# Optimization experiments

Hardware: AMD Instinct MI355X
Metric: run time of the kernel (lower is better)

## Reference

```python
import jax, jax.numpy as jnp
import numpy as np

V, E, H, L = 32000, 512, 1024, 2
B, S = 16, 128


def _gru_cell(x, h, w_ih, w_hh, b_ih, b_hh):
    # PyTorch GRUCell: gates ordered (r, z, n), chunks of size H
    gi = x @ w_ih.T + b_ih            # (B, 3H)
    gh = h @ w_hh.T + b_hh            # (B, 3H)
    i_r, i_z, i_n = jnp.split(gi, 3, axis=-1)
    h_r, h_z, h_n = jnp.split(gh, 3, axis=-1)
    r = jax.nn.sigmoid(i_r + h_r)
    z = jax.nn.sigmoid(i_z + h_z)
    n = jnp.tanh(i_n + r * h_n)
    return (1.0 - z) * n + z * h


def setup_inputs() -> dict:
    key = jax.random.key(0)
    ks = jax.random.split(key, 16)
    s = lambda fan: 1.0 / np.sqrt(fan)
    inp = {
        "hidden": jax.random.normal(ks[0], (L, B, H), jnp.float32),
        "trg": jax.random.randint(ks[1], (B, S), 0, V),
        "embedding": jax.random.normal(ks[2], (V, E), jnp.float32) * 0.02,
        # layer 0 GRU (input_size=E)
        "w_ih0": jax.random.uniform(ks[3], (3 * H, E), jnp.float32, -s(H), s(H)),
        "w_hh0": jax.random.uniform(ks[4], (3 * H, H), jnp.float32, -s(H), s(H)),
        "b_ih0": jnp.zeros((3 * H,), jnp.float32),
        "b_hh0": jnp.zeros((3 * H,), jnp.float32),
        # layer 1 GRU (input_size=H)
        "w_ih1": jax.random.uniform(ks[5], (3 * H, H), jnp.float32, -s(H), s(H)),
        "w_hh1": jax.random.uniform(ks[6], (3 * H, H), jnp.float32, -s(H), s(H)),
        "b_ih1": jnp.zeros((3 * H,), jnp.float32),
        "b_hh1": jnp.zeros((3 * H,), jnp.float32),
        # output projection MLP: Linear(H,H) -> ReLU -> Linear(H,E)
        "w1": jax.random.uniform(ks[7], (H, H), jnp.float32, -s(H), s(H)),
        "b1": jnp.zeros((H,), jnp.float32),
        "w2": jax.random.uniform(ks[8], (E, H), jnp.float32, -s(H), s(H)),
        "b2": jnp.zeros((E,), jnp.float32),
        # generator bias (weight tied to embedding)
        "b_gen": jnp.zeros((V,), jnp.float32),
    }
    return inp


def reference(hidden, trg, embedding, w_ih0, w_hh0, b_ih0, b_hh0,
              w_ih1, w_hh1, b_ih1, b_hh1, w1, b1, w2, b2, b_gen):
    def step(h, tok):
        # h: (L, B, H); tok: (B,)
        x = embedding[tok]                                 # (B, E)
        h0 = _gru_cell(x, h[0], w_ih0, w_hh0, b_ih0, b_hh0)
        h1 = _gru_cell(h0, h[1], w_ih1, w_hh1, b_ih1, b_hh1)
        new_h = jnp.stack([h0, h1], axis=0)
        out = jax.nn.relu(h1 @ w1.T + b1) @ w2.T + b2      # (B, E)
        logit = out @ embedding.T + b_gen                  # (B, V) weight-tied
        return new_h, logit

    _, logits = jax.lax.scan(step, hidden, trg.T)          # (S, B, V)
    return jnp.transpose(logits, (1, 0, 2))                # (B, S, V)
```

## Files before the change

### kernel.cpp

```cpp
#include <hip/hip_runtime.h>
#include <math.h>

#define Sn 128
#define Bn 16
#define Hn 1024
#define En 512
#define Vn 32000
#define H3 3072
#define NL0 32
#define NL1 64

typedef _Float16 h16;
typedef __attribute__((ext_vector_type(4))) _Float16 h16x4;
typedef __attribute__((ext_vector_type(8))) _Float16 h16x8;
typedef __attribute__((ext_vector_type(4))) float f32x4;

#define Q_EMB   4096000
#define Q_WIH0  (Q_EMB + 393216)
#define Q_W1    (Q_WIH0 + 262144)
#define Q_W2    (Q_W1 + 131072)
#define Q_WHH0  (Q_W2 + 786432)
#define Q_WIH1  (Q_WHH0 + 786432)
#define Q_WHH1  (Q_WIH1 + 786432)
#define Q_HID   (Q_WHH1 + 8192)
__global__ __launch_bounds__(256) void cvt_all_k(
    const float* __restrict__ emb, const float* __restrict__ wih0,
    const float* __restrict__ w1, const float* __restrict__ w2,
    const float* __restrict__ whh0, const float* __restrict__ wih1,
    const float* __restrict__ whh1, const float* __restrict__ hid,
    h16* __restrict__ E, h16* __restrict__ A, h16* __restrict__ B1,
    h16* __restrict__ B2, h16* __restrict__ D0, h16* __restrict__ D1,
    h16* __restrict__ D2, h16* __restrict__ HD)
{
  int i = blockIdx.x * 256 + threadIdx.x;
  const float* s; h16* d; int o;
  if      (i < Q_EMB)  { s = emb;  d = E;  o = i; }
  else if (i < Q_WIH0) { s = wih0; d = A;  o = i - Q_EMB; }
  else if (i < Q_W1)   { s = w1;   d = B1; o = i - Q_WIH0; }
  else if (i < Q_W2)   { s = w2;   d = B2; o = i - Q_W1; }
  else if (i < Q_WHH0) { s = whh0; d = D0; o = i - Q_W2; }
  else if (i < Q_WIH1) { s = wih1; d = D1; o = i - Q_WHH0; }
  else if (i < Q_WHH1) { s = whh1; d = D2; o = i - Q_WIH1; }
  else                 { s = hid;  d = HD; o = i - Q_WHH1; }
  float4 v = *(const float4*)(s + (size_t)o * 4);
  h16x4 ov = { (h16)v.x, (h16)v.y, (h16)v.z, (h16)v.w };
  *(h16x4*)(d + (size_t)o * 4) = ov;
}

__global__ void embed_k(const int* __restrict__ trg, const float* __restrict__ emb,
                        h16* __restrict__ Xh) {
  int t = blockIdx.x;
  int s = t >> 4, b = t & 15;
  int tok = trg[b * Sn + s];
  const float* src = emb + (size_t)tok * En;
  int e = threadIdx.x * 4;
  float4 v = *(const float4*)(src + e);
  h16x4 o = { (h16)v.x, (h16)v.y, (h16)v.z, (h16)v.w };
  *(h16x4*)(Xh + (size_t)t * En + e) = o;
}

template<int OUT_MODE, bool RELU, bool SWZ>
__global__ __launch_bounds__(256) void gemm_bt(
    const h16* __restrict__ A, const h16* __restrict__ B,
    const float* __restrict__ bias, void* __restrict__ C,
    int M, int N, int K)
{
  __shared__ h16 As[128 * 64];
  __shared__ h16 Bs[128 * 64];
  int tid = threadIdx.x;
  int l = tid & 63, wv = tid >> 6;
  int wr = wv >> 1, wc = wv & 1;

  int work = blockIdx.x;
  if (SWZ) { int q = gridDim.x >> 3; work = (work & 7) * q + (work >> 3); }
  int nMp = M >> 7;
  int brow = (work % nMp) << 7;
  int bcol = (work / nMp) << 7;

  f32x4 acc[4][4];
#pragma unroll
  for (int m = 0; m < 4; ++m)
#pragma unroll
    for (int n = 0; n < 4; ++n) acc[m][n] = (f32x4){0.f, 0.f, 0.f, 0.f};

  int nkt = K >> 6;
  for (int kt = 0; kt < nkt; ++kt) {
    const h16* Ag = A + (size_t)brow * K + kt * 64;
    const h16* Bg = B + (size_t)bcol * K + kt * 64;
#pragma unroll
    for (int c = tid; c < 2048; c += 256) {
      int half = c >> 10;
      int cc = c & 1023;
      int row = cc >> 3, slot = cc & 7;
      const h16* src = (half ? Bg : Ag) + (size_t)row * K + slot * 8;
      uint4 v = *(const uint4*)src;
      h16* dst = (half ? Bs : As) + row * 64 + ((slot ^ (row & 7)) << 3);
      *(uint4*)dst = v;
    }
    __syncthreads();
#pragma unroll
    for (int kk = 0; kk < 2; ++kk) {
      h16x8 af[4], bfr[4];
      int rb = wr * 64 + (l & 15);
      int cb2 = wc * 64 + (l & 15);
      int slot = kk * 4 + (l >> 4);
#pragma unroll
      for (int m = 0; m < 4; ++m) {
        int r = rb + m * 16;
        af[m] = *(const h16x8*)&As[r * 64 + ((slot ^ (r & 7)) << 3)];
      }
#pragma unroll
      for (int n = 0; n < 4; ++n) {
        int r = cb2 + n * 16;
        bfr[n] = *(const h16x8*)&Bs[r * 64 + ((slot ^ (r & 7)) << 3)];
      }
#pragma unroll
      for (int m = 0; m < 4; ++m)
#pragma unroll
        for (int n = 0; n < 4; ++n)
          acc[m][n] = __builtin_amdgcn_mfma_f32_16x16x32_f16(af[m], bfr[n], acc[m][n], 0, 0, 0);
    }
    __syncthreads();
  }

#pragma unroll
  for (int m = 0; m < 4; ++m) {
    int row0 = brow + wr * 64 + m * 16 + ((l >> 4) << 2);
#pragma unroll
    for (int n = 0; n < 4; ++n) {
      int col = bcol + wc * 64 + n * 16 + (l & 15);
      float bv = bias ? bias[col] : 0.f;
#pragma unroll
      for (int i = 0; i < 4; ++i) {
        int row = row0 + i;
        float v = acc[m][n][i] + bv;
        if (RELU) v = fmaxf(v, 0.f);
        if (OUT_MODE == 1) {
          ((h16*)C)[(size_t)row * N + col] = (h16)v;
        } else if (OUT_MODE == 2) {
          int rr = ((row & 15) << 7) + (row >> 4);
          ((float*)C)[(size_t)rr * N + col] = v;
        } else {
          ((float*)C)[(size_t)row * N + col] = v;
        }
      }
    }
  }
}

__global__ __launch_bounds__(256, 1) void gemm_bt256(
    const h16* __restrict__ A, const h16* __restrict__ B,
    const float* __restrict__ bias, float* __restrict__ C,
    int M, int N, int K)
{
  __shared__ h16 As[128 * 64];
  __shared__ h16 Bs[256 * 64];
  int tid = threadIdx.x;
  int l = tid & 63, wv = tid >> 6;
  int wr = wv >> 1, wc = wv & 1;

  int work = blockIdx.x;
  int q = gridDim.x >> 3; work = (work & 7) * q + (work >> 3);
  int nMp = M >> 7;
  int brow = (work % nMp) << 7;
  int bcol = (work / nMp) << 8;

  f32x4 acc[4][8];
#pragma unroll
  for (int m = 0; m < 4; ++m)
#pragma unroll
    for (int n = 0; n < 8; ++n) acc[m][n] = (f32x4){0.f, 0.f, 0.f, 0.f};

  int nkt = K >> 6;
  for (int kt = 0; kt < nkt; ++kt) {
    const h16* Ag = A + (size_t)brow * K + kt * 64;
    const h16* Bg = B + (size_t)bcol * K + kt * 64;
#pragma unroll
    for (int c = tid; c < 3072; c += 256) {
      int isB = (c >= 1024);
      int cc = isB ? (c - 1024) : c;
      int row = cc >> 3, slot = cc & 7;
      const h16* src = (isB ? Bg : Ag) + (size_t)row * K + slot * 8;
      uint4 v = *(const uint4*)src;
      h16* dst = (isB ? Bs : As) + row * 64 + ((slot ^ (row & 7)) << 3);
      *(uint4*)dst = v;
    }
    __syncthreads();
#pragma unroll
    for (int kk = 0; kk < 2; ++kk) {
      h16x8 af[4], bfr[8];
      int rb = wr * 64 + (l & 15);
      int cb2 = wc * 128 + (l & 15);
      int slot = kk * 4 + (l >> 4);
#pragma unroll
      for (int m = 0; m < 4; ++m) {
        int r = rb + m * 16;
        af[m] = *(const h16x8*)&As[r * 64 + ((slot ^ (r & 7)) << 3)];
      }
#pragma unroll
      for (int n = 0; n < 8; ++n) {
        int r = cb2 + n * 16;
        bfr[n] = *(const h16x8*)&Bs[r * 64 + ((slot ^ (r & 7)) << 3)];
      }
#pragma unroll
      for (int m = 0; m < 4; ++m)
#pragma unroll
        for (int n = 0; n < 8; ++n)
          acc[m][n] = __builtin_amdgcn_mfma_f32_16x16x32_f16(af[m], bfr[n], acc[m][n], 0, 0, 0);
    }
    __syncthreads();
  }

#pragma unroll
  for (int m = 0; m < 4; ++m) {
    int row0 = brow + wr * 64 + m * 16 + ((l >> 4) << 2);
#pragma unroll
    for (int n = 0; n < 8; ++n) {
      int col = bcol + wc * 128 + n * 16 + (l & 15);
      float bv = bias[col];
#pragma unroll
      for (int i = 0; i < 4; ++i) {
        int row = row0 + i;
        int rr = ((row & 15) << 7) + (row >> 4);
        C[(size_t)rr * N + col] = acc[m][n][i] + bv;
      }
    }
  }
}

__global__ __launch_bounds__(384, 1) void gru_mfma(
    const float* __restrict__ gi0,
    const float* __restrict__ hidden,
    const h16* __restrict__ hinit16,
    const h16* __restrict__ whh0, const float* __restrict__ bhh0,
    const h16* __restrict__ wih1, const float* __restrict__ bih1,
    const h16* __restrict__ whh1, const float* __restrict__ bhh1,
    h16* __restrict__ h0ring,
    h16* __restrict__ H1A,
    int* __restrict__ flags)
{
  __shared__ float exch[5][256];
  int bid = blockIdx.x;
  int tid = threadIdx.x;
  int w = tid >> 6, l = tid & 63;
  int li = l & 15;
  int ko = (l >> 4) << 3;
  int b0 = (l >> 4) << 2;

  __threadfence();

  int* fL0 = flags;
  int* fL1 = flags + 1024;

  if (bid < NL0) {
    int gate = w >> 1, ch = w & 1;
    int j = bid * 32 + ch * 16 + li;
    h16x8 Bf[32];
    {
      const h16* wp = whh0 + ((size_t)((gate << 10) + j) << 10) + ko;
#pragma unroll
      for (int t = 0; t < 32; ++t) Bf[t] = *(const h16x8*)(wp + t * 32);
    }
    float bR = 0.f, bZ = 0.f, bN = 0.f;
    float hprev[4];
    if (gate == 2) {
      bR = bhh0[j]; bZ = bhh0[1024 + j]; bN = bhh0[2048 + j];
#pragma unroll
      for (int i = 0; i < 4; ++i) hprev[i] = hidden[((b0 + i) << 10) + j];
    }

    for (int s = 0; s < Sn; ++s) {
      if (s > 0) {
        if (w == 0 && l < NL0)
          while (__hip_atomic_load(&fL0[l << 5], __ATOMIC_RELAXED, __HIP_MEMORY_SCOPE_AGENT) < s) {}
        __syncthreads();
        asm volatile("" ::: "memory");
      }
      float gr[4], gz[4], gn[4];
      if (gate == 2) {
        const float* gb = gi0 + ((size_t)s << 4) * H3;
#pragma unroll
        for (int i = 0; i < 4; ++i) {
          const float* g = gb + (size_t)(b0 + i) * H3 + j;
          gr[i] = g[0]; gz[i] = g[1024]; gn[i] = g[2048];
        }
      }
      const h16* hsrc = (s == 0) ? hinit16 : h0ring + (((size_t)(s - 1)) << 14);
      const h16* Ap = hsrc + (li << 10) + ko;
      f32x4 acc = (f32x4){0.f, 0.f, 0.f, 0.f};
#pragma unroll
      for (int t = 0; t < 32; ++t)
        acc = __builtin_amdgcn_mfma_f32_16x16x32_f16(*(const h16x8*)(Ap + t * 32), Bf[t], acc, 0, 0, 0);
      if (w < 4) {
#pragma unroll
        for (int i = 0; i < 4; ++i) exch[w][((b0 + i) << 4) + li] = acc[i];
      }
      __syncthreads();
      if (gate == 2) {
#pragma unroll
        for (int i = 0; i < 4; ++i) {
          int e = ((b0 + i) << 4) + li;
          float r = 1.f / (1.f + expf(-(exch[ch][e] + bR + gr[i])));
          float z = 1.f / (1.f + expf(-(exch[2 + ch][e] + bZ + gz[i])));
          float n = tanhf(gn[i] + r * (acc[i] + bN));
          float out = (1.f - z) * n + z * hprev[i];
          hprev[i] = out;
          h16 hv = (h16)out; unsigned short us; __builtin_memcpy(&us, &hv, 2);
          __hip_atomic_store((unsigned short*)h0ring + (((size_t)s) << 14) + ((b0 + i) << 10) + j,
                             us, __ATOMIC_RELAXED, __HIP_MEMORY_SCOPE_AGENT);
        }
      }
      __syncthreads();
      if (tid == 0)
        __hip_atomic_store(&fL0[bid << 5], s + 1, __ATOMIC_RELAXED, __HIP_MEMORY_SCOPE_AGENT);
    }
  } else {
    int bl = bid - NL0;
    int j = (bl << 4) + li;
    int isHH = (w >= 3);
    int gate = isHH ? (w - 3) : w;
    h16x8 Bf[32];
    {
      const h16* wsrc = isHH ? whh1 : wih1;
      const h16* wp = wsrc + ((size_t)((gate << 10) + j) << 10) + ko;
#pragma unroll
      for (int t = 0; t < 32; ++t) Bf[t] = *(const h16x8*)(wp + t * 32);
    }
    float bIR = 0.f, bIZ = 0.f, bIN = 0.f, bHR = 0.f, bHZ = 0.f, bHN = 0.f;
    float hprev[4];
    if (w == 5) {
      bIR = bih1[j]; bIZ = bih1[1024 + j]; bIN = bih1[2048 + j];
      bHR = bhh1[j]; bHZ = bhh1[1024 + j]; bHN = bhh1[2048 + j];
#pragma unroll
      for (int i = 0; i < 4; ++i) hprev[i] = hidden[16384 + ((b0 + i) << 10) + j];
    }

    for (int s = 1; s <= Sn; ++s) {
      if (w == 0) {
        if (l < NL0)
          while (__hip_atomic_load(&fL0[l << 5], __ATOMIC_RELAXED, __HIP_MEMORY_SCOPE_AGENT) < s) {}
      } else if (w == 1 && s >= 2) {
        while (__hip_atomic_load(&fL1[l << 5], __ATOMIC_RELAXED, __HIP_MEMORY_SCOPE_AGENT) < s) {}
      }
      __syncthreads();
      asm volatile("" ::: "memory");
      const h16* hsrc = isHH
          ? ((s == 1) ? hinit16 + 16384 : H1A + (((size_t)(s - 2)) << 14))
          : (h0ring + (((size_t)(s - 1)) << 14));
      const h16* Ap = hsrc + (li << 10) + ko;
      f32x4 acc = (f32x4){0.f, 0.f, 0.f, 0.f};
#pragma unroll
      for (int t = 0; t < 32; ++t)
        acc = __builtin_amdgcn_mfma_f32_16x16x32_f16(*(const h16x8*)(Ap + t * 32), Bf[t], acc, 0, 0, 0);
      if (w < 5) {
#pragma unroll
        for (int i = 0; i < 4; ++i) exch[w][((b0 + i) << 4) + li] = acc[i];
      }
      __syncthreads();
      if (w == 5) {
#pragma unroll
        for (int i = 0; i < 4; ++i) {
          int e = ((b0 + i) << 4) + li;
          float r = 1.f / (1.f + expf(-(exch[0][e] + bIR + exch[3][e] + bHR)));
          float z = 1.f / (1.f + expf(-(exch[1][e] + bIZ + exch[4][e] + bHZ)));
          float n = tanhf(exch[2][e] + bIN + r * (acc[i] + bHN));
          float out = (1.f - z) * n + z * hprev[i];
          hprev[i] = out;
          h16 hv = (h16)out; unsigned short us; __builtin_memcpy(&us, &hv, 2);
          __hip_atomic_store((unsigned short*)H1A + (((size_t)(s - 1)) << 14) + ((b0 + i) << 10) + j,
                             us, __ATOMIC_RELAXED, __HIP_MEMORY_SCOPE_AGENT);
        }
      }
      __syncthreads();
      if (tid == 0)
        __hip_atomic_store(&fL1[bl << 5], s + 1, __ATOMIC_RELAXED, __HIP_MEMORY_SCOPE_AGENT);
    }
  }
}

extern "C" void kernel_launch(void* const* d_in, const int* in_sizes, int n_in,
                              void* d_out, int out_size, void* d_ws, size_t ws_size,
                              hipStream_t stream) {
  const float* hidden = (const float*)d_in[0];
  const int*   trg    = (const int*)d_in[1];
  const float* emb    = (const float*)d_in[2];
  const float* w_ih0  = (const float*)d_in[3];
  const float* w_hh0  = (const float*)d_in[4];
  const float* b_ih0  = (const float*)d_in[5];
  const float* b_hh0  = (const float*)d_in[6];
  const float* w_ih1  = (const float*)d_in[7];
  const float* w_hh1  = (const float*)d_in[8];
  const float* b_ih1  = (const float*)d_in[9];
  const float* b_hh1  = (const float*)d_in[10];
  const float* w1     = (const float*)d_in[11];
  const float* b1     = (const float*)d_in[12];
  const float* w2     = (const float*)d_in[13];
  const float* b2     = (const float*)d_in[14];
  const float* b_gen  = (const float*)d_in[15];

  char* ws = (char*)d_ws;
  size_t off = 0;
  float* GI0    = (float*)(ws + off); off += (size_t)Sn * Bn * H3 * 4;
  h16* Xh       = (h16*)(ws + off);   off += (size_t)Sn * Bn * En * 2;
  h16* embH     = (h16*)(ws + off);   off += (size_t)Vn * En * 2;
  h16* wih0H    = (h16*)(ws + off);   off += (size_t)H3 * En * 2;
  h16* w1H      = (h16*)(ws + off);   off += (size_t)Hn * Hn * 2;
  h16* w2H      = (h16*)(ws + off);   off += (size_t)En * Hn * 2;
  h16* whh0H    = (h16*)(ws + off);   off += (size_t)H3 * Hn * 2;
  h16* wih1H    = (h16*)(ws + off);   off += (size_t)H3 * Hn * 2;
  h16* whh1H    = (h16*)(ws + off);   off += (size_t)H3 * Hn * 2;
  h16* H1A      = (h16*)(ws + off);   off += (size_t)Sn * Bn * Hn * 2;
  h16* h0ring   = (h16*)(ws + off);   off += (size_t)Sn * Bn * Hn * 2;
  h16* hinit16  = (h16*)(ws + off);   off += (size_t)2 * Bn * Hn * 2;
  int* flags    = (int*)(ws + off);   off += 16384;
  h16* Tb = (h16*)GI0;
  h16* Ub = (h16*)((char*)GI0 + (8u << 20));

  cvt_all_k<<<28320, 256, 0, stream>>>(emb, w_ih0, w1, w2, w_hh0, w_ih1, w_hh1, hidden,
                                       embH, wih0H, w1H, w2H, whh0H, wih1H, whh1H, hinit16);
  embed_k<<<Sn * Bn, 128, 0, stream>>>(trg, emb, Xh);

  gemm_bt<0, false, true><<<384, 256, 0, stream>>>(Xh, wih0H, b_ih0, GI0, Sn * Bn, H3, En);

  (void)hipMemsetAsync(flags, 0, 16384, stream);
  gru_mfma<<<NL0 + NL1, 384, 0, stream>>>(GI0, hidden, hinit16,
                                          whh0H, b_hh0, wih1H, b_ih1, whh1H, b_hh1,
                                          h0ring, H1A, flags);

  gemm_bt<1, true,  true><<<128,  256, 0, stream>>>(H1A, w1H, b1, Tb, Sn * Bn, Hn, Hn);
  gemm_bt<1, false, true><<<64,   256, 0, stream>>>(Tb, w2H, b2, Ub, Sn * Bn, En, Hn);
  gemm_bt256<<<2000, 256, 0, stream>>>(Ub, embH, b_gen, (float*)d_out, Sn * Bn, Vn, En);
}
```

Baseline: 1.488 ms.

## Fuse GRU recurrence and output head into one persistent megakernel with flag-based overlap

Merges the recurrent GRU kernel and the three head GEMMs (MLP layers and tied-embedding logits) into a single launch. Extra blocks wait on per-step layer-1 flags and per-chunk counters, so each 128-row chunk (8 timesteps) of the head computation can start while the recurrence is still running. Tb and Ub get dedicated workspace buffers instead of aliasing GI0, which is still being read. The design relies on the 96 recurrent blocks being co-resident with the spinning head blocks and on the head blocks being dispatched roughly in order. It also gives up the larger-grid GEMM tiling and runs the head GEMMs on 384-thread blocks where only 4 of the 6 waves compute.

```diff
diff --git a/kernel.cpp b/kernel.cpp
--- a/kernel.cpp
+++ b/kernel.cpp
@@ -137,9 +137,6 @@
         if (RELU) v = fmaxf(v, 0.f);
         if (OUT_MODE == 1) {
           ((h16*)C)[(size_t)row * N + col] = (h16)v;
-        } else if (OUT_MODE == 2) {
-          int rr = ((row & 15) << 7) + (row >> 4);
-          ((float*)C)[(size_t)rr * N + col] = v;
         } else {
           ((float*)C)[(size_t)row * N + col] = v;
         }
@@ -148,233 +145,354 @@
   }
 }
 
-__global__ __launch_bounds__(256, 1) void gemm_bt256(
-    const h16* __restrict__ A, const h16* __restrict__ B,
-    const float* __restrict__ bias, float* __restrict__ C,
-    int M, int N, int K)
+
+__device__ __forceinline__ void wait_fL1(int* fL1, int target, int tid) {
+  if (tid < 64) {
+    for (;;) {
+      int v = __hip_atomic_load(&fL1[tid << 5], __ATOMIC_RELAXED, __HIP_MEMORY_SCOPE_AGENT);
+      if (__all(v >= target)) break;
+      __builtin_amdgcn_s_sleep(8);
+    }
+  }
+  __syncthreads();
+  asm volatile("" ::: "memory");
+}
+
+__device__ __forceinline__ void wait_cnt(int* c, int target, int tid) {
+  if (tid == 0) {
+    while (__hip_atomic_load(c, __ATOMIC_RELAXED, __HIP_MEMORY_SCOPE_AGENT) < target)
+      __builtin_amdgcn_s_sleep(8);
+  }
+  __syncthreads();
+  asm volatile("" ::: "memory");
+}
+
+__device__ __forceinline__ void publish_cnt(int* c) {
+  __syncthreads();
+  if (threadIdx.x == 0) {
+    __threadfence();
+    atomicAdd(c, 1);
+  }
+}
+
+__device__ __forceinline__ void gemm_head128(
+    const h16* __restrict__ A, const h16* __restrict__ B, const float* __restrict__ bias,
+    h16* __restrict__ C, int ldc, int K, int relu, char* dyn, int tid)
 {
-  __shared__ h16 As[128 * 64];
-  __shared__ h16 Bs[256 * 64];
-  int tid = threadIdx.x;
+  h16* As = (h16*)dyn;
+  h16* Bs = (h16*)(dyn + 16384);
   int l = tid & 63, wv = tid >> 6;
   int wr = wv >> 1, wc = wv & 1;
-
-  int work = blockIdx.x;
-  int q = gridDim.x >> 3; work = (work & 7) * q + (work >> 3);
-  int nMp = M >> 7;
-  int brow = (work % nMp) << 7;
-  int bcol = (work / nMp) << 8;
-
-  f32x4 acc[4][8];
+  f32x4 acc[4][4];
 #pragma unroll
   for (int m = 0; m < 4; ++m)
 #pragma unroll
-    for (int n = 0; n < 8; ++n) acc[m][n] = (f32x4){0.f, 0.f, 0.f, 0.f};
-
+    for (int n = 0; n < 4; ++n) acc[m][n] = (f32x4){0.f, 0.f, 0.f, 0.f};
   int nkt = K >> 6;
   for (int kt = 0; kt < nkt; ++kt) {
-    const h16* Ag = A + (size_t)brow * K + kt * 64;
-    const h16* Bg = B + (size_t)bcol * K + kt * 64;
-#pragma unroll
-    for (int c = tid; c < 3072; c += 256) {
+    const h16* Ag = A + kt * 64;
+    const h16* Bg = B + kt * 64;
+    for (int c = tid; c < 2048; c += 384) {
+      int half = c >> 10, cc = c & 1023, row = cc >> 3, slot = cc & 7;
+      const h16* src = (half ? Bg : Ag) + (size_t)row * K + slot * 8;
+      uint4 v = *(const uint4*)src;
+      h16* dst = (half ? Bs : As) + row * 64 + ((slot ^ (row & 7)) << 3);
+      *(uint4*)dst = v;
+    }
+    __syncthreads();
+    if (wv < 4) {
+#pragma unroll
+      for (int kk = 0; kk < 2; ++kk) {
+        h16x8 af[4], bfr[4];
+        int rb = wr * 64 + (l & 15);
+        int cb2 = wc * 64 + (l & 15);
+        int slot = kk * 4 + (l >> 4);
+#pragma unroll
+        for (int m = 0; m < 4; ++m) {
+          int r = rb + m * 16;
+          af[m] = *(const h16x8*)&As[r * 64 + ((slot ^ (r & 7)) << 3)];
+        }
+#pragma unroll
+        for (int n = 0; n < 4; ++n) {
+          int r = cb2 + n * 16;
+          bfr[n] = *(const h16x8*)&Bs[r * 64 + ((slot ^ (r & 7)) << 3)];
+        }
+#pragma unroll
+        for (int m = 0; m < 4; ++m)
+#pragma unroll
+          for (int n = 0; n < 4; ++n)
+            acc[m][n] = __builtin_amdgcn_mfma_f32_16x16x32_f16(af[m], bfr[n], acc[m][n], 0, 0, 0);
+      }
+    }
+    __syncthreads();
+  }
+  if (wv < 4) {
+#pragma unroll
+    for (int m = 0; m < 4; ++m) {
+      int row0 = wr * 64 + m * 16 + ((l >> 4) << 2);
+#pragma unroll
+      for (int n = 0; n < 4; ++n) {
+        int col = wc * 64 + n * 16 + (l & 15);
+        float bv = bias[col];
+#pragma unroll
+        for (int i = 0; i < 4; ++i) {
+          float v = acc[m][n][i] + bv;
+          if (relu) v = fmaxf(v, 0.f);
+          C[(size_t)(row0 + i) * ldc + col] = (h16)v;
+        }
+      }
+    }
+  }
+}
+
+__device__ __forceinline__ void gemm_headlogit(
+    const h16* __restrict__ A, const h16* __restrict__ B, const float* __restrict__ bias,
+    float* __restrict__ C, int growbase, char* dyn, int tid)
+{
+  h16* As = (h16*)dyn;
+  h16* Bs = (h16*)(dyn + 16384);
+  int l = tid & 63, wv = tid >> 6;
+  int wr = wv >> 1, wc = wv & 1;
+  f32x4 acc[4][8];
+#pragma unroll
+  for (int m = 0; m < 4; ++m)
+#pragma unroll
+    for (int n = 0; n < 8; ++n) acc[m][n] = (f32x4){0.f, 0.f, 0.f, 0.f};
+  for (int kt = 0; kt < 8; ++kt) {
+    const h16* Ag = A + kt * 64;
+    const h16* Bg = B + kt * 64;
+    for (int c = tid; c < 3072; c += 384) {
       int isB = (c >= 1024);
       int cc = isB ? (c - 1024) : c;
       int row = cc >> 3, slot = cc & 7;
-      const h16* src = (isB ? Bg : Ag) + (size_t)row * K + slot * 8;
+      const h16* src = (isB ? Bg : Ag) + (size_t)row * 512 + slot * 8;
       uint4 v = *(const uint4*)src;
       h16* dst = (isB ? Bs : As) + row * 64 + ((slot ^ (row & 7)) << 3);
       *(uint4*)dst = v;
     }
     __syncthreads();
-#pragma unroll
-    for (int kk = 0; kk < 2; ++kk) {
-      h16x8 af[4], bfr[8];
-      int rb = wr * 64 + (l & 15);
-      int cb2 = wc * 128 + (l & 15);
-      int slot = kk * 4 + (l >> 4);
-#pragma unroll
-      for (int m = 0; m < 4; ++m) {
-        int r = rb + m * 16;
-        af[m] = *(const h16x8*)&As[r * 64 + ((slot ^ (r & 7)) << 3)];
-      }
+    if (wv < 4) {
+#pragma unroll
+      for (int kk = 0; kk < 2; ++kk) {
+        h16x8 af[4], bfr[8];
+        int rb = wr * 64 + (l & 15);
+        int cb2 = wc * 128 + (l & 15);
+        int slot = kk * 4 + (l >> 4);
+#pragma unroll
+        for (int m = 0; m < 4; ++m) {
+          int r = rb + m * 16;
+          af[m] = *(const h16x8*)&As[r * 64 + ((slot ^ (r & 7)) << 3)];
+        }
+#pragma unroll
+        for (int n = 0; n < 8; ++n) {
+          int r = cb2 + n * 16;
+          bfr[n] = *(const h16x8*)&Bs[r * 64 + ((slot ^ (r & 7)) << 3)];
+        }
+#pragma unroll
+        for (int m = 0; m < 4; ++m)
+#pragma unroll
+          for (int n = 0; n < 8; ++n)
+            acc[m][n] = __builtin_amdgcn_mfma_f32_16x16x32_f16(af[m], bfr[n], acc[m][n], 0, 0, 0);
+      }
+    }
+    __syncthreads();
+  }
+  if (wv < 4) {
+#pragma unroll
+    for (int m = 0; m < 4; ++m) {
+      int row0 = wr * 64 + m * 16 + ((l >> 4) << 2);
 #pragma unroll
       for (int n = 0; n < 8; ++n) {
-        int r = cb2 + n * 16;
-        bfr[n] = *(const h16x8*)&Bs[r * 64 + ((slot ^ (r & 7)) << 3)];
-      }
-#pragma unroll
-      for (int m = 0; m < 4; ++m)
-#pragma unroll
-        for (int n = 0; n < 8; ++n)
-          acc[m][n] = __builtin_amdgcn_mfma_f32_16x16x32_f16(af[m], bfr[n], acc[m][n], 0, 0, 0);
-    }
-    __syncthreads();
-  }
-
-#pragma unroll
-  for (int m = 0; m < 4; ++m) {
-    int row0 = brow + wr * 64 + m * 16 + ((l >> 4) << 2);
-#pragma unroll
-    for (int n = 0; n < 8; ++n) {
-      int col = bcol + wc * 128 + n * 16 + (l & 15);
-      float bv = bias[col];
-#pragma unroll
-      for (int i = 0; i < 4; ++i) {
-        int row = row0 + i;
-        int rr = ((row & 15) << 7) + (row >> 4);
-        C[(size_t)rr * N + col] = acc[m][n][i] + bv;
-      }
-    }
-  }
-}
-
-__global__ __launch_bounds__(384, 1) void gru_mfma(
+        int col = wc * 128 + n * 16 + (l & 15);
+        float bv = bias[col];
+#pragma unroll
+        for (int i = 0; i < 4; ++i) {
+          int grow = growbase + row0 + i;
+          int rr = ((grow & 15) << 7) + (grow >> 4);
+          C[(size_t)rr * Vn + col] = acc[m][n][i] + bv;
+        }
+      }
+    }
+  }
+}
+
+__global__ __launch_bounds__(384) void mega(
     const float* __restrict__ gi0,
     const float* __restrict__ hidden,
     const h16* __restrict__ hinit16,
     const h16* __restrict__ whh0, const float* __restrict__ bhh0,
     const h16* __restrict__ wih1, const float* __restrict__ bih1,
     const h16* __restrict__ whh1, const float* __restrict__ bhh1,
-    h16* __restrict__ h0ring,
-    h16* __restrict__ H1A,
-    int* __restrict__ flags)
+    h16* __restrict__ h0ring, h16* __restrict__ H1A,
+    int* __restrict__ flags,
+    const h16* __restrict__ w1H, const float* __restrict__ b1, h16* __restrict__ Tb,
+    const h16* __restrict__ w2H, const float* __restrict__ b2, h16* __restrict__ Ub,
+    const h16* __restrict__ embH, const float* __restrict__ b_gen,
+    float* __restrict__ out)
 {
-  __shared__ float exch[5][256];
+  extern __shared__ char dyn[];
   int bid = blockIdx.x;
   int tid = threadIdx.x;
-  int w = tid >> 6, l = tid & 63;
-  int li = l & 15;
-  int ko = (l >> 4) << 3;
-  int b0 = (l >> 4) << 2;
 
   __threadfence();
 
-  int* fL0 = flags;
-  int* fL1 = flags + 1024;
-
-  if (bid < NL0) {
-    int gate = w >> 1, ch = w & 1;
-    int j = bid * 32 + ch * 16 + li;
-    h16x8 Bf[32];
-    {
-      const h16* wp = whh0 + ((size_t)((gate << 10) + j) << 10) + ko;
-#pragma unroll
-      for (int t = 0; t < 32; ++t) Bf[t] = *(const h16x8*)(wp + t * 32);
-    }
-    float bR = 0.f, bZ = 0.f, bN = 0.f;
-    float hprev[4];
-    if (gate == 2) {
-      bR = bhh0[j]; bZ = bhh0[1024 + j]; bN = bhh0[2048 + j];
-#pragma unroll
-      for (int i = 0; i < 4; ++i) hprev[i] = hidden[((b0 + i) << 10) + j];
-    }
-
-    for (int s = 0; s < Sn; ++s) {
-      if (s > 0) {
-        if (w == 0 && l < NL0)
-          while (__hip_atomic_load(&fL0[l << 5], __ATOMIC_RELAXED, __HIP_MEMORY_SCOPE_AGENT) < s) {}
+  int* fL0  = flags;
+  int* fL1  = flags + 1024;
+  int* cnt1 = flags + 3072;
+  int* cnt2 = flags + 3328;
+
+  if (bid < NL0 + NL1) {
+    float* exch = (float*)dyn;
+    int w = tid >> 6, l = tid & 63;
+    int li = l & 15;
+    int ko = (l >> 4) << 3;
+    int b0 = (l >> 4) << 2;
+
+    if (bid < NL0) {
+      int gate = w >> 1, ch = w & 1;
+      int j = bid * 32 + ch * 16 + li;
+      h16x8 Bf[32];
+      {
+        const h16* wp = whh0 + ((size_t)((gate << 10) + j) << 10) + ko;
+#pragma unroll
+        for (int t = 0; t < 32; ++t) Bf[t] = *(const h16x8*)(wp + t * 32);
+      }
+      float bR = 0.f, bZ = 0.f, bN = 0.f;
+      float hprev[4];
+      if (gate == 2) {
+        bR = bhh0[j]; bZ = bhh0[1024 + j]; bN = bhh0[2048 + j];
+#pragma unroll
+        for (int i = 0; i < 4; ++i) hprev[i] = hidden[((b0 + i) << 10) + j];
+      }
+      for (int s = 0; s < Sn; ++s) {
+        if (s > 0) {
+          if (w == 0 && l < NL0)
+            while (__hip_atomic_load(&fL0[l << 5], __ATOMIC_RELAXED, __HIP_MEMORY_SCOPE_AGENT) < s) {}
+          __syncthreads();
+          asm volatile("" ::: "memory");
+        }
+        float gr[4], gz[4], gn[4];
+        if (gate == 2) {
+          const float* gb = gi0 + ((size_t)s << 4) * H3;
+#pragma unroll
+          for (int i = 0; i < 4; ++i) {
+            const float* g = gb + (size_t)(b0 + i) * H3 + j;
+            gr[i] = g[0]; gz[i] = g[1024]; gn[i] = g[2048];
+          }
+        }
+        const h16* hsrc = (s == 0) ? hinit16 : h0ring + (((size_t)(s - 1)) << 14);
+        const h16* Ap = hsrc + (li << 10) + ko;
+        f32x4 acc = (f32x4){0.f, 0.f, 0.f, 0.f};
+#pragma unroll
+        for (int t = 0; t < 32; ++t)
+          acc = __builtin_amdgcn_mfma_f32_16x16x32_f16(*(const h16x8*)(Ap + t * 32), Bf[t], acc, 0, 0, 0);
+        if (w < 4) {
+#pragma unroll
+          for (int i = 0; i < 4; ++i) exch[w * 256 + ((b0 + i) << 4) + li] = acc[i];
+        }
+        __syncthreads();
+        if (gate == 2) {
+#pragma unroll
+          for (int i = 0; i < 4; ++i) {
+            int e = ((b0 + i) << 4) + li;
+            float r = 1.f / (1.f + expf(-(exch[ch * 256 + e] + bR + gr[i])));
+            float z = 1.f / (1.f + expf(-(exch[(2 + ch) * 256 + e] + bZ + gz[i])));
+            float n = tanhf(gn[i] + r * (acc[i] + bN));
+            float o = (1.f - z) * n + z * hprev[i];
+            hprev[i] = o;
+            h16 hv = (h16)o; unsigned short us; __builtin_memcpy(&us, &hv, 2);
+            __hip_atomic_store((unsigned short*)h0ring + (((size_t)s) << 14) + ((b0 + i) << 10) + j,
+                               us, __ATOMIC_RELAXED, __HIP_MEMORY_SCOPE_AGENT);
+          }
+        }
+        __syncthreads();
+        if (tid == 0)
+          __hip_atomic_store(&fL0[bid << 5], s + 1, __ATOMIC_RELAXED, __HIP_MEMORY_SCOPE_AGENT);
+      }
+    } else {
+      int bl = bid - NL0;
+      int j = (bl << 4) + li;
+      int isHH = (w >= 3);
+      int gate = isHH ? (w - 3) : w;
+      h16x8 Bf[32];
+      {
+        const h16* wsrc = isHH ? whh1 : wih1;
+        const h16* wp = wsrc + ((size_t)((gate << 10) + j) << 10) + ko;
+#pragma unroll
+        for (int t = 0; t < 32; ++t) Bf[t] = *(const h16x8*)(wp + t * 32);
+      }
+      float bIR = 0.f, bIZ = 0.f, bIN = 0.f, bHR = 0.f, bHZ = 0.f, bHN = 0.f;
+      float hprev[4];
+      if (w == 5) {
+        bIR = bih1[j]; bIZ = bih1[1024 + j]; bIN = bih1[2048 + j];
+        bHR = bhh1[j]; bHZ = bhh1[1024 + j]; bHN = bhh1[2048 + j];
+#pragma unroll
+        for (int i = 0; i < 4; ++i) hprev[i] = hidden[16384 + ((b0 + i) << 10) + j];
+      }
+      for (int s = 1; s <= Sn; ++s) {
+        if (w == 0) {
+          if (l < NL0)
+            while (__hip_atomic_load(&fL0[l << 5], __ATOMIC_RELAXED, __HIP_MEMORY_SCOPE_AGENT) < s) {}
+        } else if (w == 1 && s >= 2) {
+          while (__hip_atomic_load(&fL1[l << 5], __ATOMIC_RELAXED, __HIP_MEMORY_SCOPE_AGENT) < s) {}
+        }
         __syncthreads();
         asm volatile("" ::: "memory");
-      }
-      float gr[4], gz[4], gn[4];
-      if (gate == 2) {
-        const float* gb = gi0 + ((size_t)s << 4) * H3;
-#pragma unroll
-        for (int i = 0; i < 4; ++i) {
-          const float* g = gb + (size_t)(b0 + i) * H3 + j;
-          gr[i] = g[0]; gz[i] = g[1024]; gn[i] = g[2048];
-        }
-      }
-      const h16* hsrc = (s == 0) ? hinit16 : h0ring + (((size_t)(s - 1)) << 14);
-      const h16* Ap = hsrc + (li << 10) + ko;
-      f32x4 acc = (f32x4){0.f, 0.f, 0.f, 0.f};
-#pragma unroll
-      for (int t = 0; t < 32; ++t)
-        acc = __builtin_amdgcn_mfma_f32_16x16x32_f16(*(const h16x8*)(Ap + t * 32), Bf[t], acc, 0, 0, 0);
-      if (w < 4) {
-#pragma unroll
-        for (int i = 0; i < 4; ++i) exch[w][((b0 + i) << 4) + li] = acc[i];
-      }
-      __syncthreads();
-      if (gate == 2) {
-#pragma unroll
-        for (int i = 0; i < 4; ++i) {
-          int e = ((b0 + i) << 4) + li;
-          float r = 1.f / (1.f + expf(-(exch[ch][e] + bR + gr[i])));
-          float z = 1.f / (1.f + expf(-(exch[2 + ch][e] + bZ + gz[i])));
-          float n = tanhf(gn[i] + r * (acc[i] + bN));
-          float out = (1.f - z) * n + z * hprev[i];
-          hprev[i] = out;
-          h16 hv = (h16)out; unsigned short us; __builtin_memcpy(&us, &hv, 2);
-          __hip_atomic_store((unsigned short*)h0ring + (((size_t)s) << 14) + ((b0 + i) << 10) + j,
-                             us, __ATOMIC_RELAXED, __HIP_MEMORY_SCOPE_AGENT);
-        }
-      }
-      __syncthreads();
-      if (tid == 0)
-        __hip_atomic_store(&fL0[bid << 5], s + 1, __ATOMIC_RELAXED, __HIP_MEMORY_SCOPE_AGENT);
-    }
+        const h16* hsrc = isHH
+            ? ((s == 1) ? hinit16 + 16384 : H1A + (((size_t)(s - 2)) << 14))
+            : (h0ring + (((size_t)(s - 1)) << 14));
+        const h16* Ap = hsrc + (li << 10) + ko;
+        f32x4 acc = (f32x4){0.f, 0.f, 0.f, 0.f};
+#pragma unroll
+        for (int t = 0; t < 32; ++t)
+          acc = __builtin_amdgcn_mfma_f32_16x16x32_f16(*(const h16x8*)(Ap + t * 32), Bf[t], acc, 0, 0, 0);
+        if (w < 5) {
+#pragma unroll
+          for (int i = 0; i < 4; ++i) exch[w * 256 + ((b0 + i) << 4) + li] = acc[i];
+        }
+        __syncthreads();
+        if (w == 5) {
+#pragma unroll
+          for (int i = 0; i < 4; ++i) {
+            int e = ((b0 + i) << 4) + li;
+            float r = 1.f / (1.f + expf(-(exch[e] + bIR + exch[768 + e] + bHR)));
+            float z = 1.f / (1.f + expf(-(exch[256 + e] + bIZ + exch[1024 + e] + bHZ)));
+            float n = tanhf(exch[512 + e] + bIN + r * (acc[i] + bHN));
+            float o = (1.f - z) * n + z * hprev[i];
+            hprev[i] = o;
+            h16 hv = (h16)o; unsigned short us; __builtin_memcpy(&us, &hv, 2);
+            __hip_atomic_store((unsigned short*)H1A + (((size_t)(s - 1)) << 14) + ((b0 + i) << 10) + j,
+                               us, __ATOMIC_RELAXED, __HIP_MEMORY_SCOPE_AGENT);
+          }
+        }
+        __syncthreads();
+        if (tid == 0)
+          __hip_atomic_store(&fL1[bl << 5], s + 1, __ATOMIC_RELAXED, __HIP_MEMORY_SCOPE_AGENT);
+      }
+    }
+    return;
+  }
+
+  int hb = bid - (NL0 + NL1);
+  int m = hb / 137;
+  int r = hb - m * 137;
+
+  if (r < 8) {
+    wait_fL1(fL1, 8 * m + 9, tid);
+    gemm_head128(H1A + (size_t)(m * 128) * Hn, w1H + (size_t)(r * 128) * Hn,
+                 b1 + r * 128, Tb + (size_t)(m * 128) * Hn + r * 128, Hn, Hn, 1, dyn, tid);
+    publish_cnt(&cnt1[m << 3]);
+  } else if (r < 12) {
+    int rn = r - 8;
+    wait_cnt(&cnt1[m << 3], 8, tid);
+    gemm_head128(Tb + (size_t)(m * 128) * Hn, w2H + (size_t)(rn * 128) * Hn,
+                 b2 + rn * 128, Ub + (size_t)(m * 128) * En + rn * 128, En, Hn, 0, dyn, tid);
+    publish_cnt(&cnt2[m << 3]);
   } else {
-    int bl = bid - NL0;
-    int j = (bl << 4) + li;
-    int isHH = (w >= 3);
-    int gate = isHH ? (w - 3) : w;
-    h16x8 Bf[32];
-    {
-      const h16* wsrc = isHH ? whh1 : wih1;
-      const h16* wp = wsrc + ((size_t)((gate << 10) + j) << 10) + ko;
-#pragma unroll
-      for (int t = 0; t < 32; ++t) Bf[t] = *(const h16x8*)(wp + t * 32);
-    }
-    float bIR = 0.f, bIZ = 0.f, bIN = 0.f, bHR = 0.f, bHZ = 0.f, bHN = 0.f;
-    float hprev[4];
-    if (w == 5) {
-      bIR = bih1[j]; bIZ = bih1[1024 + j]; bIN = bih1[2048 + j];
-      bHR = bhh1[j]; bHZ = bhh1[1024 + j]; bHN = bhh1[2048 + j];
-#pragma unroll
-      for (int i = 0; i < 4; ++i) hprev[i] = hidden[16384 + ((b0 + i) << 10) + j];
-    }
-
-    for (int s = 1; s <= Sn; ++s) {
-      if (w == 0) {
-        if (l < NL0)
-          while (__hip_atomic_load(&fL0[l << 5], __ATOMIC_RELAXED, __HIP_MEMORY_SCOPE_AGENT) < s) {}
-      } else if (w == 1 && s >= 2) {
-        while (__hip_atomic_load(&fL1[l << 5], __ATOMIC_RELAXED, __HIP_MEMORY_SCOPE_AGENT) < s) {}
-      }
-      __syncthreads();
-      asm volatile("" ::: "memory");
-      const h16* hsrc = isHH
-          ? ((s == 1) ? hinit16 + 16384 : H1A + (((size_t)(s - 2)) << 14))
-          : (h0ring + (((size_t)(s - 1)) << 14));
-      const h16* Ap = hsrc + (li << 10) + ko;
-      f32x4 acc = (f32x4){0.f, 0.f, 0.f, 0.f};
-#pragma unroll
-      for (int t = 0; t < 32; ++t)
-        acc = __builtin_amdgcn_mfma_f32_16x16x32_f16(*(const h16x8*)(Ap + t * 32), Bf[t], acc, 0, 0, 0);
-      if (w < 5) {
-#pragma unroll
-        for (int i = 0; i < 4; ++i) exch[w][((b0 + i) << 4) + li] = acc[i];
-      }
-      __syncthreads();
-      if (w == 5) {
-#pragma unroll
-        for (int i = 0; i < 4; ++i) {
-          int e = ((b0 + i) << 4) + li;
-          float r = 1.f / (1.f + expf(-(exch[0][e] + bIR + exch[3][e] + bHR)));
-          float z = 1.f / (1.f + expf(-(exch[1][e] + bIZ + exch[4][e] + bHZ)));
-          float n = tanhf(exch[2][e] + bIN + r * (acc[i] + bHN));
-          float out = (1.f - z) * n + z * hprev[i];
-          hprev[i] = out;
-          h16 hv = (h16)out; unsigned short us; __builtin_memcpy(&us, &hv, 2);
-          __hip_atomic_store((unsigned short*)H1A + (((size_t)(s - 1)) << 14) + ((b0 + i) << 10) + j,
-                             us, __ATOMIC_RELAXED, __HIP_MEMORY_SCOPE_AGENT);
-        }
-      }
-      __syncthreads();
-      if (tid == 0)
-        __hip_atomic_store(&fL1[bl << 5], s + 1, __ATOMIC_RELAXED, __HIP_MEMORY_SCOPE_AGENT);
-    }
+    int np = r - 12;
+    wait_cnt(&cnt2[m << 3], 4, tid);
+    gemm_headlogit(Ub + (size_t)(m * 128) * En, embH + (size_t)(np * 256) * En,
+                   b_gen + np * 256, out + np * 256, m * 128, dyn, tid);
   }
 }
 
@@ -412,9 +530,9 @@
   h16* H1A      = (h16*)(ws + off);   off += (size_t)Sn * Bn * Hn * 2;
   h16* h0ring   = (h16*)(ws + off);   off += (size_t)Sn * Bn * Hn * 2;
   h16* hinit16  = (h16*)(ws + off);   off += (size_t)2 * Bn * Hn * 2;
+  h16* Tb       = (h16*)(ws + off);   off += (size_t)Sn * Bn * Hn * 2;
+  h16* Ub       = (h16*)(ws + off);   off += (size_t)Sn * Bn * En * 2;
   int* flags    = (int*)(ws + off);   off += 16384;
-  h16* Tb = (h16*)GI0;
-  h16* Ub = (h16*)((char*)GI0 + (8u << 20));
 
   cvt_all_k<<<28320, 256, 0, stream>>>(emb, w_ih0, w1, w2, w_hh0, w_ih1, w_hh1, hidden,
                                        embH, wih0H, w1H, w2H, whh0H, wih1H, whh1H, hinit16);
@@ -423,11 +541,10 @@
   gemm_bt<0, false, true><<<384, 256, 0, stream>>>(Xh, wih0H, b_ih0, GI0, Sn * Bn, H3, En);
 
   (void)hipMemsetAsync(flags, 0, 16384, stream);
-  gru_mfma<<<NL0 + NL1, 384, 0, stream>>>(GI0, hidden, hinit16,
-                                          whh0H, b_hh0, wih1H, b_ih1, whh1H, b_hh1,
-                                          h0ring, H1A, flags);
-
-  gemm_bt<1, true,  true><<<128,  256, 0, stream>>>(H1A, w1H, b1, Tb, Sn * Bn, Hn, Hn);
-  gemm_bt<1, false, true><<<64,   256, 0, stream>>>(Tb, w2H, b2, Ub, Sn * Bn, En, Hn);
-  gemm_bt256<<<2000, 256, 0, stream>>>(Ub, embH, b_gen, (float*)d_out, Sn * Bn, Vn, En);
-}
+  const int LDSZ = 49152;
+  (void)hipFuncSetAttribute(reinterpret_cast<const void*>(mega),
+                            hipFuncAttributeMaxDynamicSharedMemorySize, LDSZ);
+  mega<<<NL0 + NL1 + 16 * 137, 384, LDSZ, stream>>>(
+      GI0, hidden, hinit16, whh0H, b_hh0, wih1H, b_ih1, whh1H, b_hh1,
+      h0ring, H1A, flags, w1H, b1, Tb, w2H, b2, Ub, embH, b_gen, (float*)d_out);
+}
```

After: 1.373 ms. 7.8% less time.
